# Performance work log

Measured on AMD Instinct MI355X. Metric: run time of the kernel, lower is better.

## Reference

```python
import jax, jax.numpy as jnp
import numpy as np

EPS = 1e-5  # BatchNorm eps (torch default)
PAD = 1
K = 9  # 3x3 kernel points

def conv3x3(x, w, b):
    # x: [B,C,H,W], w: [O,C,3,3]
    y = jax.lax.conv_general_dilated(x, w, (1, 1), ((PAD, PAD), (PAD, PAD)),
                                     dimension_numbers=('NCHW', 'OIHW', 'NCHW'))
    return y + b[None, :, None, None]

def deform_conv2d(x, offset, mask, weight, bias):
    # Modulated deformable conv v2, stride 1, pad 1, 3x3 kernel.
    # x: [B,C,H,W]; offset: [B,2K,H,W] (first K = dy, last K = dx); mask: [B,K,H,W]
    B, C, H, W = x.shape
    ki, kj = jnp.meshgrid(jnp.arange(3), jnp.arange(3), indexing='ij')
    ki = ki.reshape(K).astype(x.dtype)
    kj = kj.reshape(K).astype(x.dtype)
    dy = offset[:, :K].transpose(0, 2, 3, 1)   # [B,H,W,K]
    dx = offset[:, K:].transpose(0, 2, 3, 1)
    m = mask.transpose(0, 2, 3, 1)             # [B,H,W,K]
    hs = jnp.arange(H, dtype=x.dtype)
    ws = jnp.arange(W, dtype=x.dtype)
    py = hs[None, :, None, None] - PAD + ki[None, None, None, :] + dy  # [B,H,W,K]
    px = ws[None, None, :, None] - PAD + kj[None, None, None, :] + dx
    y0 = jnp.floor(py)
    x0 = jnp.floor(px)
    wy1 = py - y0
    wx1 = px - x0
    wy0 = 1.0 - wy1
    wx0 = 1.0 - wx1

    def gather(yi, xi):
        valid = ((yi >= 0) & (yi < H) & (xi >= 0) & (xi < W)).astype(x.dtype)
        yc = jnp.clip(yi, 0, H - 1).astype(jnp.int32)
        xc = jnp.clip(xi, 0, W - 1).astype(jnp.int32)
        g = jax.vmap(lambda img, yb, xb: img[:, yb, xb])(x, yc, xc)  # [B,C,H,W,K]
        return g * valid[:, None]

    val = (gather(y0, x0) * (wy0 * wx0)[:, None]
           + gather(y0, x0 + 1.0) * (wy0 * wx1)[:, None]
           + gather(y0 + 1.0, x0) * (wy1 * wx0)[:, None]
           + gather(y0 + 1.0, x0 + 1.0) * (wy1 * wx1)[:, None])
    val = val * m[:, None]  # modulation
    out = jnp.einsum('bchwk,ock->bohw', val, weight.reshape(weight.shape[0], C, K))
    return out + bias[None, :, None, None]

def dcnv2(x, w_om, b_om, w, b, gamma, beta, mean, var):
    om = conv3x3(x, w_om, b_om)               # [B,27,H,W]
    o1, o2, mr = jnp.split(om, 3, axis=1)
    offset = jnp.concatenate([o1, o2], axis=1)  # [B,18,H,W]
    mask = jax.nn.sigmoid(mr)
    y = deform_conv2d(x, offset, mask, w, b)
    scale = (gamma / jnp.sqrt(var + EPS))[None, :, None, None]
    y = (y - mean[None, :, None, None]) * scale + beta[None, :, None, None]
    return jax.nn.silu(y)

def setup_inputs() -> dict:
    key = jax.random.key(0)
    ks = jax.random.split(key, 9)
    B, C, H, W = 4, 256, 128, 128
    C4 = C // 4
    return {
        'x': jax.random.normal(ks[0], (B, C, H, W), jnp.float32),
        'w': jax.random.normal(ks[1], (4, C4, C4, 3, 3), jnp.float32) * 0.05,
        'b': jax.random.normal(ks[2], (4, C4), jnp.float32) * 0.05,
        'w_om': jax.random.normal(ks[3], (4, 27, C4, 3, 3), jnp.float32) * 0.01,
        'b_om': jax.random.normal(ks[4], (4, 27), jnp.float32) * 0.01,
        'gamma': jax.random.normal(ks[5], (4, C4), jnp.float32) * 0.1 + 1.0,
        'beta': jax.random.normal(ks[6], (4, C4), jnp.float32) * 0.1,
        'mean': jax.random.normal(ks[7], (4, C4), jnp.float32) * 0.1,
        'var': jax.random.uniform(ks[8], (4, C4), jnp.float32, minval=0.5, maxval=1.5),
    }

def reference(x, w, b, w_om, b_om, gamma, beta, mean, var):
    B, C, H, W = x.shape
    C4 = C // 4
    # channel-split into 4 independent groups, vmap identical DCNv2 over groups
    xg = x.reshape(B, 4, C4, H, W).transpose(1, 0, 2, 3, 4)  # [4,B,C4,H,W]
    yg = jax.vmap(dcnv2)(xg, w_om, b_om, w, b, gamma, beta, mean, var)
    return yg.transpose(1, 0, 2, 3, 4).reshape(B, C, H, W)
```

## Files before the change

### kernel.cpp

```cpp
#include <hip/hip_runtime.h>
#include <math.h>

#define Hs 128
#define Ws 128
#define HWs 16384

typedef __attribute__((ext_vector_type(8))) short short8;
typedef __attribute__((ext_vector_type(8))) __bf16 bf16x8;
typedef __attribute__((ext_vector_type(4))) float f32x4;
typedef __attribute__((ext_vector_type(2))) float f32x2;

static __device__ __forceinline__ float bf2f(unsigned short u) {
    union { unsigned int i; float f; } v; v.i = ((unsigned int)u) << 16; return v.f;
}
static __device__ __forceinline__ unsigned short f2bf(float f) {
    unsigned int u = __builtin_bit_cast(unsigned int, f);
    return (unsigned short)((u + 0x7fffu + ((u >> 16) & 1u)) >> 16);
}
static __device__ __forceinline__ unsigned int pack2bf(float a0, float a1) {
    return (unsigned int)f2bf(a0) | ((unsigned int)f2bf(a1) << 16);
}
static __device__ __forceinline__ f32x4 mfma16(short8 a, short8 b, f32x4 c) {
    return __builtin_amdgcn_mfma_f32_16x16x32_bf16(
        __builtin_bit_cast(bf16x8, a), __builtin_bit_cast(bf16x8, b), c, 0, 0, 0);
}
static __device__ __forceinline__ f32x2 pk_mul(f32x2 a, f32x2 b) {
    f32x2 d;
    asm("v_pk_mul_f32 %0, %1, %2" : "=v"(d) : "v"(a), "v"(b));
    return d;
}
static __device__ __forceinline__ f32x2 pk_fma(f32x2 a, f32x2 b, f32x2 c) {
    f32x2 d;
    asm("v_pk_fma_f32 %0, %1, %2, %3" : "=v"(d) : "v"(a), "v"(b), "v"(c));
    return d;
}
static __device__ __forceinline__ unsigned int cvt_pk_bf16(float lo, float hi) {
    unsigned int d;
    asm("v_cvt_pk_bf16_f32 %0, %1, %2" : "=v"(d) : "v"(lo), "v"(hi));
    return d;
}
static __device__ __forceinline__ f32x2 bfpair(unsigned int u) {
    union { unsigned int i[2]; f32x2 f; } v;
    v.i[0] = u << 16;
    v.i[1] = u & 0xffff0000u;
    return v.f;
}

__global__ __launch_bounds__(256) void k_xt(const float* __restrict__ x,
                                            const float* __restrict__ w,
                                            const float* __restrict__ b,
                                            const float* __restrict__ w_om,
                                            const float* __restrict__ gamma,
                                            const float* __restrict__ beta,
                                            const float* __restrict__ mean,
                                            const float* __restrict__ var,
                                            unsigned short* __restrict__ xT,
                                            unsigned short* __restrict__ w2,
                                            unsigned short* __restrict__ wom2,
                                            float* __restrict__ scsh) {
    const int tid = threadIdx.x;
    const int flatb = blockIdx.y * 256 + blockIdx.x;
    if (flatb < 576) {
        int idx = flatb * 256 + tid;
        if (idx < 4 * 64 * 576) {
            int go = idx / 576;
            int ck = idx - go * 576;
            int k = ck >> 6, c = ck & 63;
            w2[idx] = f2bf(w[go * 576 + c * 9 + k]);
        }
        if (idx < 4 * 32 * 576) {
            int gj = idx / 576;
            int g = gj >> 5, j = gj & 31;
            int ck = idx - gj * 576;
            int k = ck >> 6, c = ck & 63;
            float v = (j < 27) ? w_om[(g * 27 + j) * 576 + c * 9 + k] : 0.f;
            wom2[idx] = f2bf(v);
        }
        if (idx < 256) {
            float sc = gamma[idx] * rsqrtf(var[idx] + 1e-5f);
            scsh[idx] = sc;
            scsh[256 + idx] = (b[idx] - mean[idx]) * sc + beta[idx];
        }
    }

    const int img = blockIdx.y;
    const int g = img >> 2, bb = img & 3;
    const int p0 = blockIdx.x * 64;
    __shared__ float t[64 * 65];

    const float* xg = x + (size_t)(bb * 256 + g * 64) * HWs + p0;
    const int pr = tid & 63, cw = tid >> 6;
#pragma unroll
    for (int i = 0; i < 16; ++i) {
        int c = i * 4 + cw;
        t[c * 65 + pr] = xg[(size_t)c * HWs + pr];
    }
    __syncthreads();
    const int p = tid >> 2, c16 = (tid & 3) * 16;
    unsigned short* dst = xT + (size_t)img * HWs * 64 + (size_t)(p0 + p) * 64 + c16;
    unsigned int rr[8];
#pragma unroll
    for (int q = 0; q < 8; ++q)
        rr[q] = pack2bf(t[(c16 + 2 * q) * 65 + p], t[(c16 + 2 * q + 1) * 65 + p]);
    *(uint4*)dst       = make_uint4(rr[0], rr[1], rr[2], rr[3]);
    *(uint4*)(dst + 8) = make_uint4(rr[4], rr[5], rr[6], rr[7]);
}

__global__ __launch_bounds__(256, 2) void k_off(const unsigned short* __restrict__ xT,
                                                const unsigned short* __restrict__ wom2,
                                                const float* __restrict__ b_om,
                                                float* __restrict__ om) {
    const int img = blockIdx.y;
    const int g = img >> 2;
    const int h = blockIdx.x;
    const int tid = threadIdx.x;
    const int lane = tid & 63, wv = tid >> 6;
    const int mt = wv & 1, nh = wv >> 1;
    const int m = lane & 15, q = lane >> 4;

    __shared__ unsigned short xrow[3 * 130 * 72];

    const unsigned short* xTi = xT + (size_t)img * HWs * 64;
    for (int i = tid; i < 3 * 130 * 8; i += 256) {
        int rr = i / 1040;
        int rem = i - rr * 1040;
        int px = rem >> 3, j = rem & 7;
        int gh = h + rr - 1, gw = px - 1;
        uint4 v = make_uint4(0, 0, 0, 0);
        if (gh >= 0 && gh < Hs && gw >= 0 && gw < Ws)
            v = *(const uint4*)(xTi + (size_t)(gh * Ws + gw) * 64 + j * 8);
        *(uint4*)&xrow[(rr * 130 + px) * 72 + j * 8] = v;
    }

    short8 afrag[18];
    const unsigned short* wb = wom2 + (size_t)(g * 32 + mt * 16 + m) * 576 + q * 8;
#pragma unroll
    for (int t = 0; t < 18; ++t) afrag[t] = *(const short8*)(wb + t * 32);

    f32x4 acc[4];
#pragma unroll
    for (int t = 0; t < 4; ++t) acc[t] = (f32x4){0.f, 0.f, 0.f, 0.f};

    __syncthreads();

#pragma unroll
    for (int k = 0; k < 9; ++k) {
        const int ki = k / 3, kj = k - ki * 3;
#pragma unroll
        for (int s = 0; s < 2; ++s) {
#pragma unroll
            for (int t = 0; t < 4; ++t) {
                int px = (nh * 4 + t) * 16 + m + kj;
                short8 bfrag = *(const short8*)&xrow[(ki * 130 + px) * 72 + (s * 4 + q) * 8];
                acc[t] = mfma16(afrag[k * 2 + s], bfrag, acc[t]);
            }
        }
    }

    float* omi = om + (size_t)img * 27 * HWs + h * Ws;
#pragma unroll
    for (int t = 0; t < 4; ++t) {
#pragma unroll
        for (int r = 0; r < 4; ++r) {
            int j = mt * 16 + q * 4 + r;
            if (j < 27) {
                float v = acc[t][r] + b_om[g * 27 + j];
                if (j >= 18) v = 1.f / (1.f + __expf(-v));
                omi[(size_t)j * HWs + (nh * 4 + t) * 16 + m] = v;
            }
        }
    }
}

__global__ __launch_bounds__(256, 3) void k_def(const unsigned short* __restrict__ xT,
                                                const float* __restrict__ om,
                                                const unsigned short* __restrict__ w2,
                                                const float* __restrict__ scsh,
                                                float* __restrict__ out) {
    const int img = blockIdx.y;
    const int g = img >> 2, bb = img & 3;
    const int p0 = blockIdx.x * 64;
    const int tid = threadIdx.x;
    const int lane = tid & 63, wv = tid >> 6;
    const int m = lane & 15, q = lane >> 4;

    __shared__ int   pO[4][576];
    __shared__ float pW[4][576];
    __shared__ unsigned short val[2][64 * 64];
    __shared__ float lsc[64], lsh[64];

    if (tid < 64) {
        lsc[tid] = scsh[g * 64 + tid];
        lsh[tid] = scsh[256 + g * 64 + tid];
    }

    const float* omg = om + (size_t)img * 27 * HWs;
    for (int idx = tid; idx < 576; idx += 256) {
        int k = idx >> 6, pp = idx & 63;
        int p = p0 + pp;
        int h = p >> 7, w = p & 127;
        float dy = omg[k * HWs + p];
        float dx = omg[(9 + k) * HWs + p];
        float mk = omg[(18 + k) * HWs + p];
        int ki = k / 3, kj = k - ki * 3;
        float py = (float)(h - 1 + ki) + dy;
        float px = (float)(w - 1 + kj) + dx;
        float fy = floorf(py), fx = floorf(px);
        float wy1 = py - fy, wx1 = px - fx;
        float wy0 = 1.f - wy1, wx0 = 1.f - wx1;
        int y0 = (int)fy, x0 = (int)fx, y1 = y0 + 1, x1 = x0 + 1;
        bool vy0 = (y0 >= 0) && (y0 < Hs), vy1 = (y1 >= 0) && (y1 < Hs);
        bool vx0 = (x0 >= 0) && (x0 < Ws), vx1 = (x1 >= 0) && (x1 < Ws);
        int cy0 = min(max(y0, 0), Hs - 1), cy1 = min(max(y1, 0), Hs - 1);
        int cx0 = min(max(x0, 0), Ws - 1), cx1 = min(max(x1, 0), Ws - 1);
        pO[0][idx] = cy0 * Ws + cx0;
        pO[1][idx] = cy0 * Ws + cx1;
        pO[2][idx] = cy1 * Ws + cx0;
        pO[3][idx] = cy1 * Ws + cx1;
        pW[0][idx] = (vy0 && vx0) ? wy0 * wx0 * mk : 0.f;
        pW[1][idx] = (vy0 && vx1) ? wy0 * wx1 * mk : 0.f;
        pW[2][idx] = (vy1 && vx0) ? wy1 * wx0 * mk : 0.f;
        pW[3][idx] = (vy1 && vx1) ? wy1 * wx1 * mk : 0.f;
    }

    short8 afrag[18];
    const unsigned short* wb = w2 + (size_t)(g * 64 + wv * 16 + m) * 576 + q * 8;
#pragma unroll
    for (int t = 0; t < 18; ++t) afrag[t] = *(const short8*)(wb + t * 32);

    f32x4 acc[4];
#pragma unroll
    for (int t = 0; t < 4; ++t) acc[t] = (f32x4){0.f, 0.f, 0.f, 0.f};

    const unsigned short* xTi = xT + (size_t)img * HWs * 64;
    const int p = tid >> 2, c4 = tid & 3;
    const int wr_sw = ((p >> 1) & 7) << 3;
    const int rd_sw = ((m >> 1) & 7) << 3;

    __syncthreads();

    uint4 gth[2][8];
    float wfb[2][4];
    auto fetch = [&](int k, int bf) {
        const int kb = k * 64 + p;
        const int off0 = pO[0][kb], off1 = pO[1][kb], off2 = pO[2][kb], off3 = pO[3][kb];
        wfb[bf][0] = pW[0][kb]; wfb[bf][1] = pW[1][kb];
        wfb[bf][2] = pW[2][kb]; wfb[bf][3] = pW[3][kb];
        const unsigned short* s0 = xTi + (size_t)off0 * 64 + c4 * 16;
        const unsigned short* s1 = xTi + (size_t)off1 * 64 + c4 * 16;
        const unsigned short* s2 = xTi + (size_t)off2 * 64 + c4 * 16;
        const unsigned short* s3 = xTi + (size_t)off3 * 64 + c4 * 16;
        gth[bf][0] = *(const uint4*)(s0);
        gth[bf][1] = *(const uint4*)(s1);
        gth[bf][2] = *(const uint4*)(s2);
        gth[bf][3] = *(const uint4*)(s3);
        gth[bf][4] = *(const uint4*)(s0 + 8);
        gth[bf][5] = *(const uint4*)(s1 + 8);
        gth[bf][6] = *(const uint4*)(s2 + 8);
        gth[bf][7] = *(const uint4*)(s3 + 8);
    };
    fetch(0, 0);

#pragma unroll
    for (int k = 0; k < 9; ++k) {
        const int cb = k & 1, nb = cb ^ 1;
        if (k < 8) fetch(k + 1, nb);
        unsigned short* vb = &val[cb][0];
        const float* wf = wfb[cb];
        f32x2 w0p = {wf[0], wf[0]}, w1p = {wf[1], wf[1]};
        f32x2 w2p = {wf[2], wf[2]}, w3p = {wf[3], wf[3]};
#pragma unroll
        for (int it = 0; it < 2; ++it) {
            const int oc8 = (2 * c4 + it) * 8;
            unsigned int rr[4];
#pragma unroll
            for (int e = 0; e < 4; ++e) {
                f32x2 x0 = bfpair(((const unsigned int*)&gth[cb][it * 4 + 0])[e]);
                f32x2 x1 = bfpair(((const unsigned int*)&gth[cb][it * 4 + 1])[e]);
                f32x2 x2 = bfpair(((const unsigned int*)&gth[cb][it * 4 + 2])[e]);
                f32x2 x3 = bfpair(((const unsigned int*)&gth[cb][it * 4 + 3])[e]);
                f32x2 a = pk_mul(x0, w0p);
                a = pk_fma(x1, w1p, a);
                a = pk_fma(x2, w2p, a);
                a = pk_fma(x3, w3p, a);
                rr[e] = cvt_pk_bf16(a[0], a[1]);
            }
            *(uint4*)&vb[p * 64 + (oc8 ^ wr_sw)] = make_uint4(rr[0], rr[1], rr[2], rr[3]);
        }
        __syncthreads();
        const unsigned short* vr = &val[cb][0];
#pragma unroll
        for (int s = 0; s < 2; ++s) {
#pragma unroll
            for (int t = 0; t < 4; ++t) {
                const int row = t * 16 + m;
                short8 bfrag = *(const short8*)&vr[row * 64 + ((s * 32 + q * 8) ^ rd_sw)];
                acc[t] = mfma16(afrag[k * 2 + s], bfrag, acc[t]);
            }
        }
    }

    float* outg = out + ((size_t)bb * 256 + g * 64) * HWs + p0;
#pragma unroll
    for (int t = 0; t < 4; ++t) {
#pragma unroll
        for (int r = 0; r < 4; ++r) {
            int o = wv * 16 + q * 4 + r;
            float y = acc[t][r] * lsc[o] + lsh[o];
            outg[(size_t)o * HWs + t * 16 + m] = y / (1.f + __expf(-y));
        }
    }
}

extern "C" void kernel_launch(void* const* d_in, const int* in_sizes, int n_in,
                              void* d_out, int out_size, void* d_ws, size_t ws_size,
                              hipStream_t stream) {
    const float* x     = (const float*)d_in[0];
    const float* w     = (const float*)d_in[1];
    const float* b     = (const float*)d_in[2];
    const float* w_om  = (const float*)d_in[3];
    const float* b_om  = (const float*)d_in[4];
    const float* gamma = (const float*)d_in[5];
    const float* beta  = (const float*)d_in[6];
    const float* mean  = (const float*)d_in[7];
    const float* var   = (const float*)d_in[8];
    float* out = (float*)d_out;

    char* ws = (char*)d_ws;
    float* om            = (float*)ws;
    unsigned short* xT   = (unsigned short*)(ws + 28311552);
    unsigned short* w2   = (unsigned short*)(ws + 61865984);
    unsigned short* wom2 = (unsigned short*)(ws + 62160896);
    float* scsh          = (float*)(ws + 62308352);

    hipLaunchKernelGGL(k_xt, dim3(256, 16), dim3(256), 0, stream,
                       x, w, b, w_om, gamma, beta, mean, var, xT, w2, wom2, scsh);
    hipLaunchKernelGGL(k_off, dim3(128, 16), dim3(256), 0, stream, xT, wom2, b_om, om);
    hipLaunchKernelGGL(k_def, dim3(256, 16), dim3(256), 0, stream, xT, om, w2, scsh, out);
}
```

Baseline: 261.1 us.

## Remap blocks across XCDs, swizzle offset-conv LDS, vectorize transpose loads, raise occupancy

```diff
diff --git a/kernel.cpp b/kernel.cpp
--- a/kernel.cpp
+++ b/kernel.cpp
@@ -16,9 +16,6 @@
 static __device__ __forceinline__ unsigned short f2bf(float f) {
     unsigned int u = __builtin_bit_cast(unsigned int, f);
     return (unsigned short)((u + 0x7fffu + ((u >> 16) & 1u)) >> 16);
-}
-static __device__ __forceinline__ unsigned int pack2bf(float a0, float a1) {
-    return (unsigned int)f2bf(a0) | ((unsigned int)f2bf(a1) << 16);
 }
 static __device__ __forceinline__ f32x4 mfma16(short8 a, short8 b, f32x4 c) {
     return __builtin_amdgcn_mfma_f32_16x16x32_bf16(
@@ -44,6 +41,10 @@
     v.i[0] = u << 16;
     v.i[1] = u & 0xffff0000u;
     return v.f;
+}
+static __device__ __forceinline__ void xcd_map(int f, int& img, int& tile) {
+    img  = ((f & 7) << 1) | ((f >> 3) & 1);
+    tile = f >> 4;
 }
 
 __global__ __launch_bounds__(256) void k_xt(const float* __restrict__ x,
@@ -59,9 +60,9 @@
                                             unsigned short* __restrict__ wom2,
                                             float* __restrict__ scsh) {
     const int tid = threadIdx.x;
-    const int flatb = blockIdx.y * 256 + blockIdx.x;
-    if (flatb < 576) {
-        int idx = flatb * 256 + tid;
+    const int f = blockIdx.y * 256 + blockIdx.x;
+    if (f < 576) {
+        int idx = f * 256 + tid;
         if (idx < 4 * 64 * 576) {
             int go = idx / 576;
             int ck = idx - go * 576;
@@ -83,17 +84,20 @@
         }
     }
 
-    const int img = blockIdx.y;
+    int img, tile;
+    xcd_map(f, img, tile);
     const int g = img >> 2, bb = img & 3;
-    const int p0 = blockIdx.x * 64;
+    const int p0 = tile * 64;
     __shared__ float t[64 * 65];
 
     const float* xg = x + (size_t)(bb * 256 + g * 64) * HWs + p0;
-    const int pr = tid & 63, cw = tid >> 6;
-#pragma unroll
-    for (int i = 0; i < 16; ++i) {
-        int c = i * 4 + cw;
-        t[c * 65 + pr] = xg[(size_t)c * HWs + pr];
+    const int l16 = tid & 15, grp = tid >> 4;
+#pragma unroll
+    for (int pass = 0; pass < 4; ++pass) {
+        int c = pass * 16 + grp;
+        float4 v = *(const float4*)(xg + (size_t)c * HWs + l16 * 4);
+        float* tr = &t[c * 65 + l16 * 4];
+        tr[0] = v.x; tr[1] = v.y; tr[2] = v.z; tr[3] = v.w;
     }
     __syncthreads();
     const int p = tid >> 2, c16 = (tid & 3) * 16;
@@ -101,24 +105,25 @@
     unsigned int rr[8];
 #pragma unroll
     for (int q = 0; q < 8; ++q)
-        rr[q] = pack2bf(t[(c16 + 2 * q) * 65 + p], t[(c16 + 2 * q + 1) * 65 + p]);
+        rr[q] = cvt_pk_bf16(t[(c16 + 2 * q) * 65 + p], t[(c16 + 2 * q + 1) * 65 + p]);
     *(uint4*)dst       = make_uint4(rr[0], rr[1], rr[2], rr[3]);
     *(uint4*)(dst + 8) = make_uint4(rr[4], rr[5], rr[6], rr[7]);
 }
 
-__global__ __launch_bounds__(256, 2) void k_off(const unsigned short* __restrict__ xT,
+__global__ __launch_bounds__(256, 3) void k_off(const unsigned short* __restrict__ xT,
                                                 const unsigned short* __restrict__ wom2,
                                                 const float* __restrict__ b_om,
                                                 float* __restrict__ om) {
-    const int img = blockIdx.y;
+    const int f = blockIdx.y * 128 + blockIdx.x;
+    int img, h;
+    xcd_map(f, img, h);
     const int g = img >> 2;
-    const int h = blockIdx.x;
     const int tid = threadIdx.x;
     const int lane = tid & 63, wv = tid >> 6;
     const int mt = wv & 1, nh = wv >> 1;
     const int m = lane & 15, q = lane >> 4;
 
-    __shared__ unsigned short xrow[3 * 130 * 72];
+    __shared__ unsigned short xrow[3 * 130 * 64];
 
     const unsigned short* xTi = xT + (size_t)img * HWs * 64;
     for (int i = tid; i < 3 * 130 * 8; i += 256) {
@@ -129,7 +134,7 @@
         uint4 v = make_uint4(0, 0, 0, 0);
         if (gh >= 0 && gh < Hs && gw >= 0 && gw < Ws)
             v = *(const uint4*)(xTi + (size_t)(gh * Ws + gw) * 64 + j * 8);
-        *(uint4*)&xrow[(rr * 130 + px) * 72 + j * 8] = v;
+        *(uint4*)&xrow[(rr * 130 + px) * 64 + (j ^ (px & 7)) * 8] = v;
     }
 
     short8 afrag[18];
@@ -151,7 +156,8 @@
 #pragma unroll
             for (int t = 0; t < 4; ++t) {
                 int px = (nh * 4 + t) * 16 + m + kj;
-                short8 bfrag = *(const short8*)&xrow[(ki * 130 + px) * 72 + (s * 4 + q) * 8];
+                int gran = (s * 4 + q) ^ (px & 7);
+                short8 bfrag = *(const short8*)&xrow[(ki * 130 + px) * 64 + gran * 8];
                 acc[t] = mfma16(afrag[k * 2 + s], bfrag, acc[t]);
             }
         }
@@ -172,14 +178,16 @@
     }
 }
 
-__global__ __launch_bounds__(256, 3) void k_def(const unsigned short* __restrict__ xT,
+__global__ __launch_bounds__(256, 4) void k_def(const unsigned short* __restrict__ xT,
                                                 const float* __restrict__ om,
                                                 const unsigned short* __restrict__ w2,
                                                 const float* __restrict__ scsh,
                                                 float* __restrict__ out) {
-    const int img = blockIdx.y;
+    const int f = blockIdx.y * 256 + blockIdx.x;
+    int img, tile;
+    xcd_map(f, img, tile);
     const int g = img >> 2, bb = img & 3;
-    const int p0 = blockIdx.x * 64;
+    const int p0 = tile * 64;
     const int tid = threadIdx.x;
     const int lane = tid & 63, wv = tid >> 6;
     const int m = lane & 15, q = lane >> 4;
```

New measurement: 271.8 us. +4.1%, slower.
